# Optimization experiments

Measured on AMD Instinct MI355X. Metric: run time of the kernel, lower is better.

## Reference

```python
import jax, jax.numpy as jnp
import numpy as np

N, E = 50000, 800000
IN, HID, H, OUT = 128, 32, 4, 40
K_SAMPLE, EPS_K = 25.0, 1e-3  # fixed k=25 (no dp_budget), compute_beta eps


def _glorot(key, shape):
    fan_in, fan_out = shape[0], shape[-1]
    lim = jnp.sqrt(6.0 / (fan_in + fan_out))
    return jax.random.uniform(key, shape, jnp.float32, -lim, lim)


def setup_inputs() -> dict:
    key = jax.random.key(0)
    ks = jax.random.split(key, 16)
    x = jax.random.normal(ks[0], (N, IN), jnp.float32)
    edge_index = jax.random.randint(ks[1], (2, E), 0, N, jnp.int64)
    # layer 0: IN -> (H, HID)
    W0 = _glorot(ks[2], (IN, H * HID)); as0 = _glorot(ks[3], (H, HID)); ad0 = _glorot(ks[4], (H, HID)); b0 = jnp.zeros((H * HID,), jnp.float32)
    # layer 1: H*HID -> (H, HID)
    W1 = _glorot(ks[5], (H * HID, H * HID)); as1 = _glorot(ks[6], (H, HID)); ad1 = _glorot(ks[7], (H, HID)); b1 = jnp.zeros((H * HID,), jnp.float32)
    # layer 2: H*HID -> (1, OUT)
    W2 = _glorot(ks[8], (H * HID, OUT)); as2 = _glorot(ks[9], (1, OUT)); ad2 = _glorot(ks[10], (1, OUT)); b2 = jnp.zeros((OUT,), jnp.float32)
    # BatchNorm affine params (batch-stat mode, deterministic)
    g_bn0 = jnp.ones((H * HID,), jnp.float32); be_bn0 = jnp.zeros((H * HID,), jnp.float32)
    g_bn1 = jnp.ones((H * HID,), jnp.float32); be_bn1 = jnp.zeros((H * HID,), jnp.float32)
    return {"x": x, "edge_index": edge_index,
            "W0": W0, "as0": as0, "ad0": ad0, "b0": b0,
            "W1": W1, "as1": as1, "ad1": ad1, "b1": b1,
            "W2": W2, "as2": as2, "ad2": ad2, "b2": b2,
            "g_bn0": g_bn0, "be_bn0": be_bn0, "g_bn1": g_bn1, "be_bn1": be_bn1}


def gat_conv(x, src, dst, W, a_src, a_dst, bias, heads, d_out):
    # PyG GATConv, add_self_loops=False, concat over heads
    h = (x @ W).reshape(-1, heads, d_out)                       # [N,H,D]
    al_s = jnp.sum(h * a_src, axis=-1)                          # [N,H]
    al_d = jnp.sum(h * a_dst, axis=-1)                          # [N,H]
    e = jax.nn.leaky_relu(al_s[src] + al_d[dst], 0.2)           # [E,H]
    m = jax.ops.segment_max(e, dst, num_segments=N)
    m = jnp.where(jnp.isfinite(m), m, 0.0)                      # guard empty segments
    p = jnp.exp(e - m[dst])
    s = jax.ops.segment_sum(p, dst, num_segments=N)
    alpha = p / (s[dst] + 1e-16)                                # segment softmax over incoming edges
    out = jax.ops.segment_sum(alpha[:, :, None] * h[src], dst, num_segments=N)  # [N,H,D]
    return out.reshape(-1, heads * d_out) + bias


def batch_norm(x, gamma, beta):
    mu = jnp.mean(x, axis=0)
    var = jnp.mean(jnp.square(x - mu), axis=0)
    return gamma * (x - mu) * jax.lax.rsqrt(var + 1e-5) + beta


def beta_scale(l):
    return 1.0 + 1.0 / (l + 1.0) * (1.0 / (K_SAMPLE + EPS_K))


def reference(x, edge_index, W0, as0, ad0, b0, W1, as1, ad1, b1, W2, as2, ad2, b2,
              g_bn0, be_bn0, g_bn1, be_bn1):
    src, dst = edge_index[0], edge_index[1]
    h = gat_conv(x, src, dst, W0, as0, ad0, b0, H, HID)
    h = jax.nn.elu(batch_norm(h, g_bn0, be_bn0)) * beta_scale(0)
    h = gat_conv(h, src, dst, W1, as1, ad1, b1, H, HID)
    h = jax.nn.elu(batch_norm(h, g_bn1, be_bn1)) * beta_scale(1)
    h = gat_conv(h, src, dst, W2, as2, ad2, b2, 1, OUT)
    return jax.nn.log_softmax(h, axis=1)
```

## Files before the change

kernel.cpp:

```cpp
#include <hip/hip_runtime.h>
#include <math.h>

#define N_NODES 50000
#define N_EDGES 800000
#define DIN 128
#define DHID 128
#define NH 4
#define HID 32
#define DOUT 40

#define PB 128
#define NPB 391

typedef __fp16 fp16x2 __attribute__((ext_vector_type(2)));

static __device__ __forceinline__ float lrelu(float x) { return x > 0.f ? x : 0.2f * x; }

static __device__ __forceinline__ unsigned int pkh(float a, float b) {
    union { fp16x2 h2; unsigned int u; } cv;
    cv.h2 = __builtin_amdgcn_cvt_pkrtz(a, b);
    return cv.u;
}
static __device__ __forceinline__ unsigned short f2h(float a) {
    union { _Float16 h; unsigned short s; } cv;
    cv.h = (_Float16)a;
    return cv.s;
}

static __device__ __forceinline__ void fma8(float* acc, uint4 w, float p) {
    union { unsigned int u; _Float16 h[2]; } c0, c1, c2, c3;
    c0.u = w.x; c1.u = w.y; c2.u = w.z; c3.u = w.w;
    acc[0] = fmaf((float)c0.h[0], p, acc[0]);
    acc[1] = fmaf((float)c0.h[1], p, acc[1]);
    acc[2] = fmaf((float)c1.h[0], p, acc[2]);
    acc[3] = fmaf((float)c1.h[1], p, acc[3]);
    acc[4] = fmaf((float)c2.h[0], p, acc[4]);
    acc[5] = fmaf((float)c2.h[1], p, acc[5]);
    acc[6] = fmaf((float)c3.h[0], p, acc[6]);
    acc[7] = fmaf((float)c3.h[1], p, acc[7]);
}

static __device__ __forceinline__ float4 bnelu4(float4 x, float4 sc, float4 sh, float bs) {
    float y0 = fmaf(x.x, sc.x, sh.x);
    float y1 = fmaf(x.y, sc.y, sh.y);
    float y2 = fmaf(x.z, sc.z, sh.z);
    float y3 = fmaf(x.w, sc.w, sh.w);
    y0 = (y0 > 0.f ? y0 : __expf(y0) - 1.f) * bs;
    y1 = (y1 > 0.f ? y1 : __expf(y1) - 1.f) * bs;
    y2 = (y2 > 0.f ? y2 : __expf(y2) - 1.f) * bs;
    y3 = (y3 > 0.f ? y3 : __expf(y3) - 1.f) * bs;
    return {y0, y1, y2, y3};
}

__global__ __launch_bounds__(256) void bucket_hist_kernel(const int* __restrict__ dstv, int* __restrict__ bhist) {
    __shared__ int h[PB];
    if (threadIdx.x < PB) h[threadIdx.x] = 0;
    __syncthreads();
    for (int i = blockIdx.x * blockDim.x + threadIdx.x; i < N_EDGES; i += gridDim.x * blockDim.x)
        atomicAdd(&h[(unsigned)dstv[i] / NPB], 1);
    __syncthreads();
    if (threadIdx.x < PB) atomicAdd(&bhist[threadIdx.x], h[threadIdx.x]);
}

__global__ __launch_bounds__(128) void bucket_scan_kernel(const int* __restrict__ bhist,
                                                          int* __restrict__ bucket_base, int* __restrict__ cursor) {
    __shared__ int sA[PB], sB[PB];
    int t = threadIdx.x;
    sA[t] = bhist[t];
    __syncthreads();
    int* s = sA; int* d2 = sB;
    for (int off = 1; off < PB; off <<= 1) {
        d2[t] = s[t] + (t >= off ? s[t - off] : 0);
        __syncthreads();
        int* tmp = s; s = d2; d2 = tmp;
    }
    int excl = s[t] - bhist[t];
    bucket_base[t] = excl;
    cursor[t] = excl;
    if (t == PB - 1) bucket_base[PB] = s[t];
}

__global__ __launch_bounds__(256) void partition_kernel(const int* __restrict__ srcv, const int* __restrict__ dstv,
                                                        int* __restrict__ cursor, uint2* __restrict__ part) {
    __shared__ uint2 rec[2048];
    __shared__ int cnt[PB], lofs[PB], gbase[PB];
    __shared__ int sA[PB], sB[PB];
    __shared__ int tot_s;
    const int t = threadIdx.x;
    const int base0 = blockIdx.x * 4096;
    for (int round = 0; round < 2; ++round) {
        int rbase = base0 + round * 2048;
        if (t < PB) cnt[t] = 0;
        __syncthreads();
        int myb[8]; int myr[8]; uint2 myrec[8];
#pragma unroll
        for (int i = 0; i < 8; ++i) {
            int e = rbase + i * 256 + t;
            bool valid = e < N_EDGES;
            int sv = valid ? srcv[e] : 0;
            int dv = valid ? dstv[e] : 0;
            myrec[i].x = (unsigned)sv;
            myrec[i].y = (unsigned)dv;
            int b = (unsigned)dv / NPB;
            myb[i] = valid ? b : -1;
            myr[i] = valid ? atomicAdd(&cnt[b], 1) : 0;
        }
        __syncthreads();
        if (t < PB) sA[t] = cnt[t];
        __syncthreads();
        int* s = sA; int* d2 = sB;
        for (int off = 1; off < PB; off <<= 1) {
            if (t < PB) d2[t] = s[t] + (t >= off ? s[t - off] : 0);
            __syncthreads();
            int* tmp = s; s = d2; d2 = tmp;
        }
        if (t < PB) {
            int c = cnt[t];
            lofs[t] = s[t] - c;
            gbase[t] = c > 0 ? atomicAdd(&cursor[t], c) : 0;
            if (t == PB - 1) tot_s = s[t];
        }
        __syncthreads();
#pragma unroll
        for (int i = 0; i < 8; ++i)
            if (myb[i] >= 0) rec[lofs[myb[i]] + myr[i]] = myrec[i];
        __syncthreads();
        int tot = tot_s;
#pragma unroll
        for (int i = 0; i < 8; ++i) {
            int lp = i * 256 + t;
            if (lp < tot) {
                uint2 r = rec[lp];
                int b = r.y / NPB;
                part[gbase[b] + (lp - lofs[b])] = r;
            }
        }
        __syncthreads();
    }
}

__global__ __launch_bounds__(256) void bucket_csr_kernel(const uint2* __restrict__ part, const int* __restrict__ bucket_base,
                                                         int* __restrict__ row_ptr, int* __restrict__ csr_src) {
    __shared__ int hist[512], sA[512], sB[512], cur[NPB];
    const int b = blockIdx.x, t = threadIdx.x;
    const int base = bucket_base[b];
    const int n = bucket_base[b + 1] - base;
    hist[t] = 0; hist[t + 256] = 0;
    __syncthreads();
    for (int i = t; i < n; i += 256)
        atomicAdd(&hist[part[base + i].y - b * NPB], 1);
    __syncthreads();
    sA[t] = hist[t]; sA[t + 256] = hist[t + 256];
    __syncthreads();
    int* s = sA; int* d2 = sB;
    for (int off = 1; off < 512; off <<= 1) {
        d2[t] = s[t] + (t >= off ? s[t - off] : 0);
        int u = t + 256;
        d2[u] = s[u] + (u >= off ? s[u - off] : 0);
        __syncthreads();
        int* tmp = s; s = d2; d2 = tmp;
    }
    for (int j = t; j < NPB; j += 256) {
        int node = b * NPB + j;
        int excl = s[j] - hist[j];
        if (node < N_NODES) row_ptr[node] = base + excl;
        cur[j] = excl;
    }
    if (b == PB - 1 && t == 0) row_ptr[N_NODES] = N_EDGES;
    __syncthreads();
    for (int i = t; i < n; i += 256) {
        uint2 r = part[base + i];
        int loc = r.y - b * NPB;
        int p = atomicAdd(&cur[loc], 1);
        csr_src[base + p] = (int)r.x;
    }
}

__global__ __launch_bounds__(256) void gemm128_kernel(
    const float* __restrict__ X, const float* __restrict__ W,
    const float* __restrict__ a_src, const float* __restrict__ a_dst,
    const float* __restrict__ scale, const float* __restrict__ shift, float bscale, int apply_bn,
    unsigned int* __restrict__ Hout, float* __restrict__ als, float* __restrict__ ald) {
    __shared__ float Xs[32][68];
    __shared__ float Ws[32][64];
    const int t = threadIdx.x;
    const int tx = t & 15, ty = t >> 4;
    const int r0 = (blockIdx.x >> 1) * 64;
    const int c0 = (blockIdx.x & 1) * 64;
    const int sr = t >> 2, sa = t & 3;
    const int wk = t >> 4, wc = (t & 15) * 4;

    int gr = r0 + sr; gr = gr < N_NODES ? gr : N_NODES - 1;
    const float* Xrow = X + (size_t)gr * 128;
    float4 xpreA = *(const float4*)(Xrow + 8 * sa);
    float4 xpreB = *(const float4*)(Xrow + 8 * sa + 4);
    if (apply_bn) {
        xpreA = bnelu4(xpreA, *(const float4*)(scale + 8 * sa), *(const float4*)(shift + 8 * sa), bscale);
        xpreB = bnelu4(xpreB, *(const float4*)(scale + 8 * sa + 4), *(const float4*)(shift + 8 * sa + 4), bscale);
    }
    float4 wpreA = *(const float4*)(W + (size_t)wk * 128 + c0 + wc);
    float4 wpreB = *(const float4*)(W + (size_t)(wk + 16) * 128 + c0 + wc);

    float acc[4][4];
#pragma unroll
    for (int i = 0; i < 4; ++i)
#pragma unroll
        for (int c = 0; c < 4; ++c) acc[i][c] = 0.f;

    for (int step = 0; step < 4; ++step) {
        __syncthreads();
        Xs[8 * sa + 0][sr] = xpreA.x;
        Xs[8 * sa + 1][sr] = xpreA.y;
        Xs[8 * sa + 2][sr] = xpreA.z;
        Xs[8 * sa + 3][sr] = xpreA.w;
        Xs[8 * sa + 4][sr] = xpreB.x;
        Xs[8 * sa + 5][sr] = xpreB.y;
        Xs[8 * sa + 6][sr] = xpreB.z;
        Xs[8 * sa + 7][sr] = xpreB.w;
        *(float4*)&Ws[wk][wc] = wpreA;
        *(float4*)&Ws[wk + 16][wc] = wpreB;
        if (step < 3) {
            int k0 = (step + 1) * 32;
            xpreA = *(const float4*)(Xrow + k0 + 8 * sa);
            xpreB = *(const float4*)(Xrow + k0 + 8 * sa + 4);
            if (apply_bn) {
                xpreA = bnelu4(xpreA, *(const float4*)(scale + k0 + 8 * sa), *(const float4*)(shift + k0 + 8 * sa), bscale);
                xpreB = bnelu4(xpreB, *(const float4*)(scale + k0 + 8 * sa + 4), *(const float4*)(shift + k0 + 8 * sa + 4), bscale);
            }
            wpreA = *(const float4*)(W + (size_t)(k0 + wk) * 128 + c0 + wc);
            wpreB = *(const float4*)(W + (size_t)(k0 + wk + 16) * 128 + c0 + wc);
        }
        __syncthreads();
#pragma unroll
        for (int kk = 0; kk < 32; ++kk) {
            float4 xv = *(const float4*)&Xs[kk][4 * ty];
            float4 wv = *(const float4*)&Ws[kk][4 * tx];
            float xr[4] = {xv.x, xv.y, xv.z, xv.w};
            float wr[4] = {wv.x, wv.y, wv.z, wv.w};
#pragma unroll
            for (int i = 0; i < 4; ++i)
#pragma unroll
                for (int c = 0; c < 4; ++c)
                    acc[i][c] = fmaf(xr[i], wr[c], acc[i][c]);
        }
    }
    const int head = (c0 >> 5) + (tx >> 3);
    float asv[4], adv[4];
#pragma unroll
    for (int c = 0; c < 4; ++c) {
        asv[c] = a_src[(head & 1) * 32 + (4 * tx + c) % 32 + (head >> 1) * 64];
        adv[c] = a_dst[(head & 1) * 32 + (4 * tx + c) % 32 + (head >> 1) * 64];
    }
#pragma unroll
    for (int i = 0; i < 4; ++i) {
        int r = r0 + 4 * ty + i;
        bool valid = r < N_NODES;
        if (valid) {
            uint2 pk = {pkh(acc[i][0], acc[i][1]), pkh(acc[i][2], acc[i][3])};
            *(uint2*)(Hout + (size_t)r * 64 + (c0 >> 1) + 2 * tx) = pk;
        }
        float ps = 0.f, pd = 0.f;
#pragma unroll
        for (int c = 0; c < 4; ++c) {
            ps = fmaf(acc[i][c], asv[c], ps);
            pd = fmaf(acc[i][c], adv[c], pd);
        }
#pragma unroll
        for (int off = 1; off < 8; off <<= 1) {
            ps += __shfl_xor(ps, off);
            pd += __shfl_xor(pd, off);
        }
        if (valid && (tx & 7) == 0) {
            als[r * 4 + head] = ps;
            ald[r * 4 + head] = pd;
        }
    }
}

__global__ __launch_bounds__(256) void gemm40_kernel(
    const float* __restrict__ X, const float* __restrict__ W,
    const float* __restrict__ a_src, const float* __restrict__ a_dst,
    const float* __restrict__ scale, const float* __restrict__ shift, float bscale,
    unsigned short* __restrict__ Hout, float* __restrict__ als, float* __restrict__ ald) {
    __shared__ float Xs[64][36];
    __shared__ float Ws[40][36];
    const int t = threadIdx.x;
    const int tx = t & 7, ty = t >> 3;
    const int r0 = blockIdx.x * 64;
    const int sr = t >> 2, sa = t & 3;

    int gr = r0 + sr; gr = gr < N_NODES ? gr : N_NODES - 1;
    const float* Xrow = X + (size_t)gr * 128;
    float4 xpreA = bnelu4(*(const float4*)(Xrow + 8 * sa),
                          *(const float4*)(scale + 8 * sa), *(const float4*)(shift + 8 * sa), bscale);
    float4 xpreB = bnelu4(*(const float4*)(Xrow + 8 * sa + 4),
                          *(const float4*)(scale + 8 * sa + 4), *(const float4*)(shift + 8 * sa + 4), bscale);
    float wpre[5];
#pragma unroll
    for (int i = 0; i < 5; ++i) wpre[i] = W[t + 256 * i];

    float acc[2][5];
#pragma unroll
    for (int i = 0; i < 2; ++i)
#pragma unroll
        for (int j = 0; j < 5; ++j) acc[i][j] = 0.f;

    for (int step = 0; step < 4; ++step) {
        __syncthreads();
        *(float4*)&Xs[sr][8 * sa] = xpreA;
        *(float4*)&Xs[sr][8 * sa + 4] = xpreB;
#pragma unroll
        for (int i = 0; i < 5; ++i) {
            int idx = t + 256 * i;
            Ws[idx % 40][idx / 40] = wpre[i];
        }
        if (step < 3) {
            int k0 = (step + 1) * 32;
            xpreA = bnelu4(*(const float4*)(Xrow + k0 + 8 * sa),
                           *(const float4*)(scale + k0 + 8 * sa), *(const float4*)(shift + k0 + 8 * sa), bscale);
            xpreB = bnelu4(*(const float4*)(Xrow + k0 + 8 * sa + 4),
                           *(const float4*)(scale + k0 + 8 * sa + 4), *(const float4*)(shift + k0 + 8 * sa + 4), bscale);
#pragma unroll
            for (int i = 0; i < 5; ++i) wpre[i] = W[k0 * 40 + t + 256 * i];
        }
        __syncthreads();
#pragma unroll
        for (int kk4 = 0; kk4 < 8; ++kk4) {
            float4 xa = *(const float4*)&Xs[2 * ty][4 * kk4];
            float4 xb = *(const float4*)&Xs[2 * ty + 1][4 * kk4];
#pragma unroll
            for (int j = 0; j < 5; ++j) {
                float4 wv = *(const float4*)&Ws[tx + 8 * j][4 * kk4];
                acc[0][j] = fmaf(xa.x, wv.x, acc[0][j]);
                acc[0][j] = fmaf(xa.y, wv.y, acc[0][j]);
                acc[0][j] = fmaf(xa.z, wv.z, acc[0][j]);
                acc[0][j] = fmaf(xa.w, wv.w, acc[0][j]);
                acc[1][j] = fmaf(xb.x, wv.x, acc[1][j]);
                acc[1][j] = fmaf(xb.y, wv.y, acc[1][j]);
                acc[1][j] = fmaf(xb.z, wv.z, acc[1][j]);
                acc[1][j] = fmaf(xb.w, wv.w, acc[1][j]);
            }
        }
    }
    float asv[5], adv[5];
#pragma unroll
    for (int j = 0; j < 5; ++j) {
        asv[j] = a_src[tx + 8 * j];
        adv[j] = a_dst[tx + 8 * j];
    }
#pragma unroll
    for (int i = 0; i < 2; ++i) {
        int r = r0 + 2 * ty + i;
        bool valid = r < N_NODES;
        if (valid) {
#pragma unroll
            for (int j = 0; j < 5; ++j)
                Hout[(size_t)r * 40 + tx + 8 * j] = f2h(acc[i][j]);
        }
        float ps = 0.f, pd = 0.f;
#pragma unroll
        for (int j = 0; j < 5; ++j) {
            ps = fmaf(acc[i][j], asv[j], ps);
            pd = fmaf(acc[i][j], adv[j], pd);
        }
#pragma unroll
        for (int off = 1; off < 8; off <<= 1) {
            ps += __shfl_xor(ps, off);
            pd += __shfl_xor(pd, off);
        }
        if (valid && tx == 0) {
            als[r] = ps;
            ald[r] = pd;
        }
    }
}

__global__ __launch_bounds__(256) void agg128_kernel(
    const int* __restrict__ row_ptr, const int* __restrict__ csr_src,
    const unsigned int* __restrict__ Ht, const float* __restrict__ als, const float* __restrict__ ald,
    const float* __restrict__ bias, float* __restrict__ out) {
    __shared__ float s_p[4][256];
    __shared__ int s_u[4][64];
    int v = (blockIdx.x * blockDim.x + threadIdx.x) >> 6;
    v = __builtin_amdgcn_readfirstlane(v);
    int lane = threadIdx.x & 63;
    int wslot = threadIdx.x >> 6;
    if (v >= N_NODES) return;
    int beg = row_ptr[v], end = row_ptr[v + 1];
    float4 ad4 = *(const float4*)(ald + (size_t)v * 4);
    const int g = lane >> 4;
    const int li = lane & 15;
    const int hh = li >> 2;
    float tsum = 0.f;
    float acc[8];
#pragma unroll
    for (int j = 0; j < 8; ++j) acc[j] = 0.f;

    for (int cbeg = beg; cbeg < end; cbeg += 64) {
        int cnt = min(64, end - cbeg);
        bool act = lane < cnt;
        int u = act ? csr_src[cbeg + lane] : 0;
        float p0, p1, p2, p3;
        if (act) {
            float4 s4 = *(const float4*)(als + (size_t)u * 4);
            p0 = __expf(lrelu(s4.x + ad4.x));
            p1 = __expf(lrelu(s4.y + ad4.y));
            p2 = __expf(lrelu(s4.z + ad4.z));
            p3 = __expf(lrelu(s4.w + ad4.w));
        } else {
            p0 = p1 = p2 = p3 = 0.f;
        }
        s_u[wslot][lane] = u;
        float4 pv = {p0, p1, p2, p3};
        *(float4*)&s_p[wslot][lane * 4] = pv;
        for (int i = 0; i < cnt; i += 8) {
            int ea = i + g;
            int eb = i + 4 + g;
            int ua = s_u[wslot][ea];
            int ub = s_u[wslot][eb];
            float pa = s_p[wslot][ea * 4 + hh];
            float pb = s_p[wslot][eb * 4 + hh];
            uint4 wa = *(const uint4*)(Ht + (size_t)ua * 64 + li * 4);
            uint4 wb = *(const uint4*)(Ht + (size_t)ub * 64 + li * 4);
            tsum += pa + pb;
            fma8(acc, wa, pa);
            fma8(acc, wb, pb);
        }
    }
#pragma unroll
    for (int j = 0; j < 8; ++j) {
        acc[j] += __shfl_xor(acc[j], 16);
        acc[j] += __shfl_xor(acc[j], 32);
    }
    tsum += __shfl_xor(tsum, 16);
    tsum += __shfl_xor(tsum, 32);
    float inv = 1.f / (tsum + 1e-16f);
    if (g == 0) {
        float4 b0 = *(const float4*)(bias + 8 * li);
        float4 b1 = *(const float4*)(bias + 8 * li + 4);
        float4 o0 = {acc[0] * inv + b0.x, acc[1] * inv + b0.y, acc[2] * inv + b0.z, acc[3] * inv + b0.w};
        float4 o1 = {acc[4] * inv + b1.x, acc[5] * inv + b1.y, acc[6] * inv + b1.z, acc[7] * inv + b1.w};
        *(float4*)(out + (size_t)v * DHID + 8 * li) = o0;
        *(float4*)(out + (size_t)v * DHID + 8 * li + 4) = o1;
    }
}

__global__ __launch_bounds__(256) void agg40_kernel(
    const int* __restrict__ row_ptr, const int* __restrict__ csr_src,
    const uint4* __restrict__ Ht4, const float* __restrict__ als, const float* __restrict__ ald,
    const float* __restrict__ bias, float* __restrict__ out) {
    __shared__ float s_p[4][76];
    __shared__ int s_u[4][76];
    __shared__ float s_red[4][12][41];
    int v = (blockIdx.x * blockDim.x + threadIdx.x) >> 6;
    v = __builtin_amdgcn_readfirstlane(v);
    int lane = threadIdx.x & 63;
    int wslot = threadIdx.x >> 6;
    if (v >= N_NODES) return;
    int beg = row_ptr[v], end = row_ptr[v + 1];
    float adv = ald[v];
    const int g = lane / 5;
    const int li = lane - g * 5;
    const bool gact = lane < 60;
    if (lane < 12) { s_u[wslot][64 + lane] = 0; s_p[wslot][64 + lane] = 0.f; }
    float tsum = 0.f;
    float a[8];
#pragma unroll
    for (int j = 0; j < 8; ++j) a[j] = 0.f;

    for (int cbeg = beg; cbeg < end; cbeg += 64) {
        int cnt = min(64, end - cbeg);
        bool act = lane < cnt;
        int u = act ? csr_src[cbeg + lane] : 0;
        float p = act ? __expf(lrelu(als[u] + adv)) : 0.f;
        s_u[wslot][lane] = u;
        s_p[wslot][lane] = p;
        for (int i = 0; i < cnt; i += 12) {
            int e = i + g;
            int uu = s_u[wslot][e];
            float pp = s_p[wslot][e];
            uint4 w = {0u, 0u, 0u, 0u};
            if (gact) w = Ht4[(size_t)uu * 5 + li];
            if (gact) tsum += pp;
            fma8(a, w, pp);
        }
    }
    if (gact) {
#pragma unroll
        for (int j = 0; j < 8; ++j) s_red[wslot][g][li * 8 + j] = a[j];
        if (li == 0) s_red[wslot][g][40] = tsum;
    }
    bool fown = lane < DOUT;
    float accf = 0.f, T = 0.f;
#pragma unroll
    for (int g2 = 0; g2 < 12; ++g2) {
        if (fown) accf += s_red[wslot][g2][lane];
        T += s_red[wslot][g2][40];
    }
    float inv = 1.f / (T + 1e-16f);
    float z = fown ? (accf * inv + bias[lane]) : -1e30f;
    float zm = z;
#pragma unroll
    for (int off = 1; off < 64; off <<= 1) zm = fmaxf(zm, __shfl_xor(zm, off));
    float se = fown ? __expf(z - zm) : 0.f;
#pragma unroll
    for (int off = 1; off < 64; off <<= 1) se += __shfl_xor(se, off);
    float ls = zm + logf(se);
    if (fown) out[(size_t)v * DOUT + lane] = z - ls;
}

__global__ __launch_bounds__(256) void bn_stats_kernel(const float* __restrict__ X,
                                                       float* __restrict__ sums, float* __restrict__ sqs) {
    const int t = threadIdx.x;
    const int tid = blockIdx.x * 256 + t;
    const float4* X4 = (const float4*)X;
    float4 s = {0.f, 0.f, 0.f, 0.f}, q = {0.f, 0.f, 0.f, 0.f};
    for (int i = tid; i < N_NODES * 32; i += 500 * 256) {
        float4 vv = X4[i];
        s.x += vv.x; s.y += vv.y; s.z += vv.z; s.w += vv.w;
        q.x += vv.x * vv.x; q.y += vv.y * vv.y; q.z += vv.z * vv.z; q.w += vv.w * vv.w;
    }
    __shared__ float ls[1024], lq[1024];
    *(float4*)&ls[t * 4] = s;
    *(float4*)&lq[t * 4] = q;
    __syncthreads();
    if (t < 128) {
        int c4 = t >> 2, j = t & 3;
        float S = 0.f, Q = 0.f;
#pragma unroll
        for (int k = 0; k < 8; ++k) {
            S += ls[(c4 + 32 * k) * 4 + j];
            Q += lq[(c4 + 32 * k) * 4 + j];
        }
        atomicAdd(&sums[t], S);
        atomicAdd(&sqs[t], Q);
    }
}

__global__ void bn_finalize_kernel(const float* __restrict__ sums, const float* __restrict__ sqs,
                                   const float* __restrict__ gamma, const float* __restrict__ beta,
                                   float* __restrict__ scale, float* __restrict__ shift) {
    int f = threadIdx.x;
    if (f < DHID) {
        float mu = sums[f] * (1.f / N_NODES);
        float var = sqs[f] * (1.f / N_NODES) - mu * mu;
        float sc = gamma[f] * rsqrtf(var + 1e-5f);
        scale[f] = sc;
        shift[f] = beta[f] - mu * sc;
    }
}

extern "C" void kernel_launch(void* const* d_in, const int* in_sizes, int n_in,
                              void* d_out, int out_size, void* d_ws, size_t ws_size,
                              hipStream_t stream) {
    (void)in_sizes; (void)n_in; (void)out_size; (void)ws_size;
    const float* x = (const float*)d_in[0];
    const int* ei = (const int*)d_in[1];
    const float* W0 = (const float*)d_in[2];
    const float* as0 = (const float*)d_in[3];
    const float* ad0 = (const float*)d_in[4];
    const float* b0 = (const float*)d_in[5];
    const float* W1 = (const float*)d_in[6];
    const float* as1 = (const float*)d_in[7];
    const float* ad1 = (const float*)d_in[8];
    const float* b1 = (const float*)d_in[9];
    const float* W2 = (const float*)d_in[10];
    const float* as2 = (const float*)d_in[11];
    const float* ad2 = (const float*)d_in[12];
    const float* b2 = (const float*)d_in[13];
    const float* g_bn0 = (const float*)d_in[14];
    const float* be_bn0 = (const float*)d_in[15];
    const float* g_bn1 = (const float*)d_in[16];
    const float* be_bn1 = (const float*)d_in[17];
    float* out = (float*)d_out;

    const int* srcv = ei;
    const int* dstv = ei + N_EDGES;

    char* p = (char*)d_ws;
    auto carve = [&](size_t bytes) {
        char* q = p;
        p += (bytes + 255) & ~(size_t)255;
        return q;
    };
    unsigned int* h_bf = (unsigned int*)carve((size_t)N_NODES * 64 * 4);
    float* agg   = (float*)carve((size_t)N_NODES * DHID * 4);
    float* als   = (float*)carve((size_t)N_NODES * NH * 4);
    float* ald   = (float*)carve((size_t)N_NODES * NH * 4);
    int* row_ptr = (int*)carve((size_t)(N_NODES + 1) * 4);
    int* csr_src = (int*)carve((size_t)N_EDGES * 4);
    uint2* part  = (uint2*)carve((size_t)N_EDGES * 8);
    int* bhist   = (int*)carve(PB * 4);
    int* bucket_base = (int*)carve((PB + 1) * 4);
    int* cursor  = (int*)carve(PB * 4);
    float* sums  = (float*)carve(256 * 4);
    float* sqs   = sums + 128;
    float* scale = (float*)carve(DHID * 4);
    float* shift = (float*)carve(DHID * 4);

    const float bs0 = 1.0f + 1.0f / 25.001f;
    const float bs1 = 1.0f + 0.5f / 25.001f;

    const int RT64 = (N_NODES + 63) / 64;
    const int G128B = RT64 * 2;
    const int G40B = RT64;
    const int AB = (N_NODES * 64 + 255) / 256;
    const int PARTB = (N_EDGES + 4095) / 4096;

    hipMemsetAsync(bhist, 0, PB * 4, stream);
    bucket_hist_kernel<<<400, 256, 0, stream>>>(dstv, bhist);
    bucket_scan_kernel<<<1, PB, 0, stream>>>(bhist, bucket_base, cursor);
    partition_kernel<<<PARTB, 256, 0, stream>>>(srcv, dstv, cursor, part);
    bucket_csr_kernel<<<PB, 256, 0, stream>>>(part, bucket_base, row_ptr, csr_src);

    gemm128_kernel<<<G128B, 256, 0, stream>>>(x, W0, as0, ad0, nullptr, nullptr, 1.f, 0, h_bf, als, ald);
    agg128_kernel<<<AB, 256, 0, stream>>>(row_ptr, csr_src, h_bf, als, ald, b0, agg);
    hipMemsetAsync(sums, 0, 256 * 4, stream);
    bn_stats_kernel<<<500, 256, 0, stream>>>(agg, sums, sqs);
    bn_finalize_kernel<<<1, 128, 0, stream>>>(sums, sqs, g_bn0, be_bn0, scale, shift);

    gemm128_kernel<<<G128B, 256, 0, stream>>>(agg, W1, as1, ad1, scale, shift, bs0, 1, h_bf, als, ald);
    agg128_kernel<<<AB, 256, 0, stream>>>(row_ptr, csr_src, h_bf, als, ald, b1, agg);
    hipMemsetAsync(sums, 0, 256 * 4, stream);
    bn_stats_kernel<<<500, 256, 0, stream>>>(agg, sums, sqs);
    bn_finalize_kernel<<<1, 128, 0, stream>>>(sums, sqs, g_bn1, be_bn1, scale, shift);

    gemm40_kernel<<<G40B, 256, 0, stream>>>(agg, W2, as2, ad2, scale, shift, bs1, (unsigned short*)h_bf, als, ald);
    agg40_kernel<<<AB, 256, 0, stream>>>(row_ptr, csr_src, (const uint4*)h_bf, als, ald, b2, out);
}
```

Before: 271.9 us.

## Fold BN finalize into GEMM prologue, pack edge records, merge memsets

Removes the two single-block bn_finalize launches by having each GEMM block compute BN scale/shift from the raw sums into shared memory. The two per-layer memsets are merged into the initial bhist memset by giving each layer its own sums buffer. Partition records are packed into one 32-bit word (src<<16 | dst), which halves the partition traffic. That packing only works for node ids below 65536; N=50000 fits for src, but dst also needs 16 bits, which it has here. The cost is some redundant per-block finalize math.

```diff
diff --git a/kernel.cpp b/kernel.cpp
--- a/kernel.cpp
+++ b/kernel.cpp
@@ -81,8 +81,8 @@
 }
 
 __global__ __launch_bounds__(256) void partition_kernel(const int* __restrict__ srcv, const int* __restrict__ dstv,
-                                                        int* __restrict__ cursor, uint2* __restrict__ part) {
-    __shared__ uint2 rec[2048];
+                                                        int* __restrict__ cursor, unsigned* __restrict__ part) {
+    __shared__ unsigned rec[2048];
     __shared__ int cnt[PB], lofs[PB], gbase[PB];
     __shared__ int sA[PB], sB[PB];
     __shared__ int tot_s;
@@ -92,15 +92,14 @@
         int rbase = base0 + round * 2048;
         if (t < PB) cnt[t] = 0;
         __syncthreads();
-        int myb[8]; int myr[8]; uint2 myrec[8];
+        int myb[8]; int myr[8]; unsigned myrec[8];
 #pragma unroll
         for (int i = 0; i < 8; ++i) {
             int e = rbase + i * 256 + t;
             bool valid = e < N_EDGES;
             int sv = valid ? srcv[e] : 0;
             int dv = valid ? dstv[e] : 0;
-            myrec[i].x = (unsigned)sv;
-            myrec[i].y = (unsigned)dv;
+            myrec[i] = ((unsigned)sv << 16) | (unsigned)dv;
             int b = (unsigned)dv / NPB;
             myb[i] = valid ? b : -1;
             myr[i] = valid ? atomicAdd(&cnt[b], 1) : 0;
@@ -130,8 +129,8 @@
         for (int i = 0; i < 8; ++i) {
             int lp = i * 256 + t;
             if (lp < tot) {
-                uint2 r = rec[lp];
-                int b = r.y / NPB;
+                unsigned r = rec[lp];
+                int b = (r & 0xFFFFu) / NPB;
                 part[gbase[b] + (lp - lofs[b])] = r;
             }
         }
@@ -139,7 +138,7 @@
     }
 }
 
-__global__ __launch_bounds__(256) void bucket_csr_kernel(const uint2* __restrict__ part, const int* __restrict__ bucket_base,
+__global__ __launch_bounds__(256) void bucket_csr_kernel(const unsigned* __restrict__ part, const int* __restrict__ bucket_base,
                                                          int* __restrict__ row_ptr, int* __restrict__ csr_src) {
     __shared__ int hist[512], sA[512], sB[512], cur[NPB];
     const int b = blockIdx.x, t = threadIdx.x;
@@ -148,7 +147,7 @@
     hist[t] = 0; hist[t + 256] = 0;
     __syncthreads();
     for (int i = t; i < n; i += 256)
-        atomicAdd(&hist[part[base + i].y - b * NPB], 1);
+        atomicAdd(&hist[(part[base + i] & 0xFFFFu) - b * NPB], 1);
     __syncthreads();
     sA[t] = hist[t]; sA[t + 256] = hist[t + 256];
     __syncthreads();
@@ -169,20 +168,22 @@
     if (b == PB - 1 && t == 0) row_ptr[N_NODES] = N_EDGES;
     __syncthreads();
     for (int i = t; i < n; i += 256) {
-        uint2 r = part[base + i];
-        int loc = r.y - b * NPB;
+        unsigned r = part[base + i];
+        int loc = (int)(r & 0xFFFFu) - b * NPB;
         int p = atomicAdd(&cur[loc], 1);
-        csr_src[base + p] = (int)r.x;
+        csr_src[base + p] = (int)(r >> 16);
     }
 }
 
 __global__ __launch_bounds__(256) void gemm128_kernel(
     const float* __restrict__ X, const float* __restrict__ W,
     const float* __restrict__ a_src, const float* __restrict__ a_dst,
-    const float* __restrict__ scale, const float* __restrict__ shift, float bscale, int apply_bn,
+    const float* __restrict__ sums, const float* __restrict__ sqs,
+    const float* __restrict__ gamma, const float* __restrict__ beta, float bscale, int apply_bn,
     unsigned int* __restrict__ Hout, float* __restrict__ als, float* __restrict__ ald) {
     __shared__ float Xs[32][68];
     __shared__ float Ws[32][64];
+    __shared__ float scale_s[DHID], shift_s[DHID];
     const int t = threadIdx.x;
     const int tx = t & 15, ty = t >> 4;
     const int r0 = (blockIdx.x >> 1) * 64;
@@ -190,13 +191,22 @@
     const int sr = t >> 2, sa = t & 3;
     const int wk = t >> 4, wc = (t & 15) * 4;
 
+    if (apply_bn && t < DHID) {
+        float mu = sums[t] * (1.f / N_NODES);
+        float var = sqs[t] * (1.f / N_NODES) - mu * mu;
+        float sc = gamma[t] * rsqrtf(var + 1e-5f);
+        scale_s[t] = sc;
+        shift_s[t] = beta[t] - mu * sc;
+    }
+    __syncthreads();
+
     int gr = r0 + sr; gr = gr < N_NODES ? gr : N_NODES - 1;
     const float* Xrow = X + (size_t)gr * 128;
     float4 xpreA = *(const float4*)(Xrow + 8 * sa);
     float4 xpreB = *(const float4*)(Xrow + 8 * sa + 4);
     if (apply_bn) {
-        xpreA = bnelu4(xpreA, *(const float4*)(scale + 8 * sa), *(const float4*)(shift + 8 * sa), bscale);
-        xpreB = bnelu4(xpreB, *(const float4*)(scale + 8 * sa + 4), *(const float4*)(shift + 8 * sa + 4), bscale);
+        xpreA = bnelu4(xpreA, *(const float4*)(scale_s + 8 * sa), *(const float4*)(shift_s + 8 * sa), bscale);
+        xpreB = bnelu4(xpreB, *(const float4*)(scale_s + 8 * sa + 4), *(const float4*)(shift_s + 8 * sa + 4), bscale);
     }
     float4 wpreA = *(const float4*)(W + (size_t)wk * 128 + c0 + wc);
     float4 wpreB = *(const float4*)(W + (size_t)(wk + 16) * 128 + c0 + wc);
@@ -224,8 +234,8 @@
             xpreA = *(const float4*)(Xrow + k0 + 8 * sa);
             xpreB = *(const float4*)(Xrow + k0 + 8 * sa + 4);
             if (apply_bn) {
-                xpreA = bnelu4(xpreA, *(const float4*)(scale + k0 + 8 * sa), *(const float4*)(shift + k0 + 8 * sa), bscale);
-                xpreB = bnelu4(xpreB, *(const float4*)(scale + k0 + 8 * sa + 4), *(const float4*)(shift + k0 + 8 * sa + 4), bscale);
+                xpreA = bnelu4(xpreA, *(const float4*)(scale_s + k0 + 8 * sa), *(const float4*)(shift_s + k0 + 8 * sa), bscale);
+                xpreB = bnelu4(xpreB, *(const float4*)(scale_s + k0 + 8 * sa + 4), *(const float4*)(shift_s + k0 + 8 * sa + 4), bscale);
             }
             wpreA = *(const float4*)(W + (size_t)(k0 + wk) * 128 + c0 + wc);
             wpreB = *(const float4*)(W + (size_t)(k0 + wk + 16) * 128 + c0 + wc);
@@ -280,21 +290,32 @@
 __global__ __launch_bounds__(256) void gemm40_kernel(
     const float* __restrict__ X, const float* __restrict__ W,
     const float* __restrict__ a_src, const float* __restrict__ a_dst,
-    const float* __restrict__ scale, const float* __restrict__ shift, float bscale,
+    const float* __restrict__ sums, const float* __restrict__ sqs,
+    const float* __restrict__ gamma, const float* __restrict__ beta, float bscale,
     unsigned short* __restrict__ Hout, float* __restrict__ als, float* __restrict__ ald) {
     __shared__ float Xs[64][36];
     __shared__ float Ws[40][36];
+    __shared__ float scale_s[DHID], shift_s[DHID];
     const int t = threadIdx.x;
     const int tx = t & 7, ty = t >> 3;
     const int r0 = blockIdx.x * 64;
     const int sr = t >> 2, sa = t & 3;
 
+    if (t < DHID) {
+        float mu = sums[t] * (1.f / N_NODES);
+        float var = sqs[t] * (1.f / N_NODES) - mu * mu;
+        float sc = gamma[t] * rsqrtf(var + 1e-5f);
+        scale_s[t] = sc;
+        shift_s[t] = beta[t] - mu * sc;
+    }
+    __syncthreads();
+
     int gr = r0 + sr; gr = gr < N_NODES ? gr : N_NODES - 1;
     const float* Xrow = X + (size_t)gr * 128;
     float4 xpreA = bnelu4(*(const float4*)(Xrow + 8 * sa),
-                          *(const float4*)(scale + 8 * sa), *(const float4*)(shift + 8 * sa), bscale);
+                          *(const float4*)(scale_s + 8 * sa), *(const float4*)(shift_s + 8 * sa), bscale);
     float4 xpreB = bnelu4(*(const float4*)(Xrow + 8 * sa + 4),
-                          *(const float4*)(scale + 8 * sa + 4), *(const float4*)(shift + 8 * sa + 4), bscale);
+                          *(const float4*)(scale_s + 8 * sa + 4), *(const float4*)(shift_s + 8 * sa + 4), bscale);
     float wpre[5];
 #pragma unroll
     for (int i = 0; i < 5; ++i) wpre[i] = W[t + 256 * i];
@@ -317,9 +338,9 @@
         if (step < 3) {
             int k0 = (step + 1) * 32;
             xpreA = bnelu4(*(const float4*)(Xrow + k0 + 8 * sa),
-                           *(const float4*)(scale + k0 + 8 * sa), *(const float4*)(shift + k0 + 8 * sa), bscale);
+                           *(const float4*)(scale_s + k0 + 8 * sa), *(const float4*)(shift_s + k0 + 8 * sa), bscale);
             xpreB = bnelu4(*(const float4*)(Xrow + k0 + 8 * sa + 4),
-                           *(const float4*)(scale + k0 + 8 * sa + 4), *(const float4*)(shift + k0 + 8 * sa + 4), bscale);
+                           *(const float4*)(scale_s + k0 + 8 * sa + 4), *(const float4*)(shift_s + k0 + 8 * sa + 4), bscale);
 #pragma unroll
             for (int i = 0; i < 5; ++i) wpre[i] = W[k0 * 40 + t + 256 * i];
         }
@@ -534,19 +555,6 @@
         }
         atomicAdd(&sums[t], S);
         atomicAdd(&sqs[t], Q);
-    }
-}
-
-__global__ void bn_finalize_kernel(const float* __restrict__ sums, const float* __restrict__ sqs,
-                                   const float* __restrict__ gamma, const float* __restrict__ beta,
-                                   float* __restrict__ scale, float* __restrict__ shift) {
-    int f = threadIdx.x;
-    if (f < DHID) {
-        float mu = sums[f] * (1.f / N_NODES);
-        float var = sqs[f] * (1.f / N_NODES) - mu * mu;
-        float sc = gamma[f] * rsqrtf(var + 1e-5f);
-        scale[f] = sc;
-        shift[f] = beta[f] - mu * sc;
     }
 }
 
@@ -589,14 +597,14 @@
     float* ald   = (float*)carve((size_t)N_NODES * NH * 4);
     int* row_ptr = (int*)carve((size_t)(N_NODES + 1) * 4);
     int* csr_src = (int*)carve((size_t)N_EDGES * 4);
-    uint2* part  = (uint2*)carve((size_t)N_EDGES * 8);
-    int* bhist   = (int*)carve(PB * 4);
+    unsigned* part = (unsigned*)carve((size_t)N_EDGES * 4);
+    int* bhist   = (int*)carve((PB + 512) * 4);
+    float* sums0 = (float*)(bhist + PB);
+    float* sqs0  = sums0 + 128;
+    float* sums1 = sqs0 + 128;
+    float* sqs1  = sums1 + 128;
     int* bucket_base = (int*)carve((PB + 1) * 4);
     int* cursor  = (int*)carve(PB * 4);
-    float* sums  = (float*)carve(256 * 4);
-    float* sqs   = sums + 128;
-    float* scale = (float*)carve(DHID * 4);
-    float* shift = (float*)carve(DHID * 4);
 
     const float bs0 = 1.0f + 1.0f / 25.001f;
     const float bs1 = 1.0f + 0.5f / 25.001f;
@@ -607,24 +615,20 @@
     const int AB = (N_NODES * 64 + 255) / 256;
     const int PARTB = (N_EDGES + 4095) / 4096;
 
-    hipMemsetAsync(bhist, 0, PB * 4, stream);
+    hipMemsetAsync(bhist, 0, (PB + 512) * 4, stream);
     bucket_hist_kernel<<<400, 256, 0, stream>>>(dstv, bhist);
     bucket_scan_kernel<<<1, PB, 0, stream>>>(bhist, bucket_base, cursor);
     partition_kernel<<<PARTB, 256, 0, stream>>>(srcv, dstv, cursor, part);
     bucket_csr_kernel<<<PB, 256, 0, stream>>>(part, bucket_base, row_ptr, csr_src);
 
-    gemm128_kernel<<<G128B, 256, 0, stream>>>(x, W0, as0, ad0, nullptr, nullptr, 1.f, 0, h_bf, als, ald);
+    gemm128_kernel<<<G128B, 256, 0, stream>>>(x, W0, as0, ad0, nullptr, nullptr, nullptr, nullptr, 1.f, 0, h_bf, als, ald);
     agg128_kernel<<<AB, 256, 0, stream>>>(row_ptr, csr_src, h_bf, als, ald, b0, agg);
-    hipMemsetAsync(sums, 0, 256 * 4, stream);
-    bn_stats_kernel<<<500, 256, 0, stream>>>(agg, sums, sqs);
-    bn_finalize_kernel<<<1, 128, 0, stream>>>(sums, sqs, g_bn0, be_bn0, scale, shift);
-
-    gemm128_kernel<<<G128B, 256, 0, stream>>>(agg, W1, as1, ad1, scale, shift, bs0, 1, h_bf, als, ald);
+    bn_stats_kernel<<<500, 256, 0, stream>>>(agg, sums0, sqs0);
+
+    gemm128_kernel<<<G128B, 256, 0, stream>>>(agg, W1, as1, ad1, sums0, sqs0, g_bn0, be_bn0, bs0, 1, h_bf, als, ald);
     agg128_kernel<<<AB, 256, 0, stream>>>(row_ptr, csr_src, h_bf, als, ald, b1, agg);
-    hipMemsetAsync(sums, 0, 256 * 4, stream);
-    bn_stats_kernel<<<500, 256, 0, stream>>>(agg, sums, sqs);
-    bn_finalize_kernel<<<1, 128, 0, stream>>>(sums, sqs, g_bn1, be_bn1, scale, shift);
-
-    gemm40_kernel<<<G40B, 256, 0, stream>>>(agg, W2, as2, ad2, scale, shift, bs1, (unsigned short*)h_bf, als, ald);
+    bn_stats_kernel<<<500, 256, 0, stream>>>(agg, sums1, sqs1);
+
+    gemm40_kernel<<<G40B, 256, 0, stream>>>(agg, W2, as2, ad2, sums1, sqs1, g_bn1, be_bn1, bs1, (unsigned short*)h_bf, als, ald);
     agg40_kernel<<<AB, 256, 0, stream>>>(row_ptr, csr_src, (const uint4*)h_bf, als, ald, b2, out);
 }
```

Result: no change. 270.1 us, median of 2 (-0.6%).
